# Kernel optimization log

Hardware: AMD Instinct MI355X
Metric: run time of the kernel (lower is better)

Reference implementation:

```python
import jax, jax.numpy as jnp
import numpy as np

B, T, D = 16, 32, 4096
H, HD = 32, 128          # n_heads, head_dim
MAX_SEQ = 2048
START_POS = 1024


def _rope(x):
    # x: [b, t, h, hd]; faithful to source: positions start at 0 (no start_pos offset)
    t, hd = x.shape[1], x.shape[-1]
    theta = 10000.0 ** (-2.0 * jnp.arange(0, hd, 2, dtype=jnp.float32) / hd)  # [hd/2]
    freqs = jnp.arange(t, dtype=jnp.float32)[:, None] * theta                 # [t, hd/2]
    cos = jnp.repeat(jnp.cos(freqs), 2, axis=-1)[None, :, None, :]            # [1,t,1,hd]
    sin = jnp.repeat(jnp.sin(freqs), 2, axis=-1)[None, :, None, :]
    # rotate: even slots <- -odd, odd slots <- even (interleaved)
    x_rot = jnp.stack([-x[..., 1::2], x[..., 0::2]], axis=-1).reshape(x.shape)
    return x * cos + x_rot * sin


def setup_inputs() -> dict:
    key = jax.random.key(0)
    ks = jax.random.split(key, 7)
    s = 0.02
    return {
        "x": jax.random.normal(ks[0], (B, T, D), dtype=jnp.float32),
        "wq": jax.random.normal(ks[1], (D, D), dtype=jnp.float32) * s,
        "wk": jax.random.normal(ks[2], (D, D), dtype=jnp.float32) * s,
        "wv": jax.random.normal(ks[3], (D, D), dtype=jnp.float32) * s,
        "wo": jax.random.normal(ks[4], (D, D), dtype=jnp.float32) * s,
        "k_cache": jax.random.normal(ks[5], (B, MAX_SEQ, H, HD), dtype=jnp.float32),
        "v_cache": jax.random.normal(ks[6], (B, MAX_SEQ, H, HD), dtype=jnp.float32),
        "start_pos": START_POS,
    }


def reference(x, wq, wk, wv, wo, k_cache, v_cache, start_pos):
    b, t, _ = x.shape
    xq = (x @ wq).reshape(b, t, H, HD)
    xk = (x @ wk).reshape(b, t, H, HD)
    xv = (x @ wv).reshape(b, t, H, HD)
    xq = _rope(xq)
    xk = _rope(xk)
    # KV-cache append (start_pos is a static Python int)
    k_cache = jax.lax.dynamic_update_slice(k_cache, xk, (0, start_pos, 0, 0))
    v_cache = jax.lax.dynamic_update_slice(v_cache, xv, (0, start_pos, 0, 0))
    L = start_pos + t
    keys = k_cache[:, :L]    # [b, L, h, hd]
    values = v_cache[:, :L]
    # n_rep == 1 -> repeat_kv is identity
    scores = jnp.einsum("bthd,bshd->bhts", xq, keys) / np.float32(np.sqrt(HD))
    probs = jax.nn.softmax(scores.astype(jnp.float32), axis=-1).astype(xq.dtype)
    out = jnp.einsum("bhts,bshd->bthd", probs, values).reshape(b, t, H * HD)
    return out @ wo
```

## Files before the change

kernel.cpp:

```cpp
#include <hip/hip_runtime.h>
#include <hip/hip_bf16.h>

#define B_ 16
#define T_ 32
#define D_ 4096
#define H_ 32
#define HD_ 128
#define MAXS_ 2048
#define M_ (B_*T_)

typedef __hip_bfloat16 bf16;
typedef __attribute__((ext_vector_type(8))) short bf16x8;
typedef __attribute__((ext_vector_type(4))) float f32x4;

static __device__ __forceinline__ short f2b(float f) {
    bf16 h = __float2bfloat16(f);
    return *reinterpret_cast<short*>(&h);
}
static __device__ __forceinline__ float b2f(short s) {
    bf16 h;
    *reinterpret_cast<short*>(&h) = s;
    return __bfloat162float(h);
}

#define GLD16(gsrc, ldst) \
    __builtin_amdgcn_global_load_lds((const __attribute__((address_space(1))) void*)(gsrc), \
        (__attribute__((address_space(3))) void*)(ldst), 16, 0, 0)

__global__ __launch_bounds__(256) void conv_x(const float* __restrict__ x, bf16* __restrict__ xb) {
    int idx = blockIdx.x * 256 + threadIdx.x;
    const float4* xf = (const float4*)x;
    float4 a = xf[idx * 2], b = xf[idx * 2 + 1];
    bf16x8 o;
    o[0] = f2b(a.x); o[1] = f2b(a.y); o[2] = f2b(a.z); o[3] = f2b(a.w);
    o[4] = f2b(b.x); o[5] = f2b(b.y); o[6] = f2b(b.z); o[7] = f2b(b.w);
    *(bf16x8*)&xb[(size_t)idx * 8] = o;
}

__global__ __launch_bounds__(256) void transpose_w(const float* __restrict__ W, bf16* __restrict__ wt) {
    __shared__ float Ts[64][65];
    const int n0 = blockIdx.x * 64, k0 = blockIdx.y * 64;
    const int t = threadIdx.x;
    {
        int kk = t >> 4, nn = (t & 15) * 4;
        #pragma unroll
        for (int r = 0; r < 4; ++r) {
            float4 v = *(const float4*)&W[(size_t)(k0 + kk + 16 * r) * D_ + n0 + nn];
            Ts[kk + 16 * r][nn + 0] = v.x;
            Ts[kk + 16 * r][nn + 1] = v.y;
            Ts[kk + 16 * r][nn + 2] = v.z;
            Ts[kk + 16 * r][nn + 3] = v.w;
        }
    }
    __syncthreads();
    const int kg = t & 7, nr = t >> 3;
    #pragma unroll
    for (int r = 0; r < 2; ++r) {
        int n = nr + 32 * r;
        bf16x8 o;
        #pragma unroll
        for (int j = 0; j < 8; ++j) o[j] = f2b(Ts[kg * 8 + j][n]);
        *(bf16x8*)&wt[(size_t)(n0 + n) * D_ + k0 + kg * 8] = o;
    }
}

__global__ __launch_bounds__(256) void gemm_qkvw(const bf16* __restrict__ A,
        const float* __restrict__ wq, const float* __restrict__ wk,
        const float* __restrict__ wv, bf16* __restrict__ out) {
    const int K = D_;
    const int wsel = blockIdx.x >> 5;
    const float* W = (wsel == 0) ? wq : (wsel == 1) ? wk : wv;
    const int lcol0 = (blockIdx.x & 31) * 128;
    bf16* Ob = out + (size_t)wsel * M_ * D_;
    __shared__ bf16 As[2][64 * 32];
    __shared__ short Bs[2][128][40];
    const int tid = threadIdx.x, lane = tid & 63, wave = tid >> 6;
    const int wr = wave >> 1, wc = wave & 1;
    const int lg = lane >> 4, li = lane & 15;
    const int row0 = blockIdx.y * 64;
    const int bq = tid & 31, kq = tid >> 5;
    f32x4 acc[2][4];
    #pragma unroll
    for (int i = 0; i < 2; ++i)
        #pragma unroll
        for (int j = 0; j < 4; ++j)
            #pragma unroll
            for (int r = 0; r < 4; ++r) acc[i][j][r] = 0.f;

    const int sw = (li & 3) << 4;
    for (int k0 = 0; k0 < K; k0 += 64) {
        float4 wv4[2][4];
        #pragma unroll
        for (int h = 0; h < 2; ++h)
            #pragma unroll
            for (int i = 0; i < 4; ++i)
                wv4[h][i] = *(const float4*)&W[(size_t)(k0 + 32 * h + kq * 4 + i) * D_ + lcol0 + bq * 4];
        {
            int X = tid * 16;
            int row = X >> 6;
            int kb = (X & 63) ^ ((row & 3) << 4);
            GLD16(A + (size_t)(row0 + row) * K + k0 + (kb >> 1),      (char*)As[0] + wave * 1024);
            GLD16(A + (size_t)(row0 + row) * K + k0 + 32 + (kb >> 1), (char*)As[1] + wave * 1024);
        }
        #pragma unroll
        for (int h = 0; h < 2; ++h)
            #pragma unroll
            for (int j = 0; j < 4; ++j) {
                int n = bq * 4 + j;
                short4 col;
                col.x = f2b(((const float*)&wv4[h][0])[j]);
                col.y = f2b(((const float*)&wv4[h][1])[j]);
                col.z = f2b(((const float*)&wv4[h][2])[j]);
                col.w = f2b(((const float*)&wv4[h][3])[j]);
                *(short4*)((char*)&Bs[h][n][0] + ((kq * 8) ^ (((n >> 4) & 3) << 4))) = col;
            }
        __syncthreads();
        bf16x8 af[2][2], bfr[2][4];
        #pragma unroll
        for (int h = 0; h < 2; ++h) {
            #pragma unroll
            for (int i = 0; i < 2; ++i) {
                int row = wr * 32 + i * 16 + li;
                af[h][i] = *(const bf16x8*)((const char*)As[h] + row * 64 + ((lg * 16) ^ sw));
            }
            #pragma unroll
            for (int j = 0; j < 4; ++j) {
                int row = wc * 64 + j * 16 + li;
                bfr[h][j] = *(const bf16x8*)((const char*)&Bs[h][row][0] + ((lg * 16) ^ (((row >> 4) & 3) << 4)));
            }
        }
        #pragma unroll
        for (int h = 0; h < 2; ++h)
            #pragma unroll
            for (int i = 0; i < 2; ++i)
                #pragma unroll
                for (int j = 0; j < 4; ++j)
                    acc[i][j] = __builtin_amdgcn_mfma_f32_16x16x32_bf16(af[h][i], bfr[h][j], acc[i][j], 0, 0, 0);
        __syncthreads();
    }
    #pragma unroll
    for (int i = 0; i < 2; ++i)
        for (int j = 0; j < 4; ++j)
            for (int r = 0; r < 4; ++r) {
                int row = row0 + wr * 32 + i * 16 + lg * 4 + r;
                int col = lcol0 + wc * 64 + j * 16 + li;
                Ob[(size_t)row * D_ + col] = __float2bfloat16(acc[i][j][r]);
            }
}

template<int BM, int BN>
__global__ __launch_bounds__(256) void gemm_bf16t(const bf16* __restrict__ A,
        const bf16* __restrict__ Bt, float* __restrict__ O) {
    constexpr int IM = BM / 32;
    constexpr int JN = BN / 32;
    constexpr int nA = (BM * 64) / 4096;
    constexpr int nB = (BN * 64) / 4096;
    const int K = D_;
    __shared__ bf16 As[2][BM * 32];
    __shared__ bf16 Bs[2][BN * 32];
    const int tid = threadIdx.x, lane = tid & 63, wave = tid >> 6;
    const int wr = wave >> 1, wc = wave & 1;
    const int lg = lane >> 4, li = lane & 15;
    const int row0 = blockIdx.y * BM, col0 = blockIdx.x * BN;
    f32x4 acc[IM][JN];
    #pragma unroll
    for (int i = 0; i < IM; ++i)
        #pragma unroll
        for (int j = 0; j < JN; ++j)
            #pragma unroll
            for (int r = 0; r < 4; ++r) acc[i][j][r] = 0.f;

    const int sw = (li & 3) << 4;
    for (int k0 = 0; k0 < K; k0 += 64) {
        #pragma unroll
        for (int h = 0; h < 2; ++h) {
            #pragma unroll
            for (int i = 0; i < nA; ++i) {
                int X = (i * 256 + tid) * 16;
                int row = X >> 6;
                int kb = (X & 63) ^ ((row & 3) << 4);
                GLD16(A + (size_t)(row0 + row) * K + k0 + 32 * h + (kb >> 1),
                      (char*)As[h] + (i * 256 + wave * 64) * 16);
            }
            #pragma unroll
            for (int i = 0; i < nB; ++i) {
                int X = (i * 256 + tid) * 16;
                int row = X >> 6;
                int kb = (X & 63) ^ ((row & 3) << 4);
                GLD16(Bt + (size_t)(col0 + row) * K + k0 + 32 * h + (kb >> 1),
                      (char*)Bs[h] + (i * 256 + wave * 64) * 16);
            }
        }
        __syncthreads();
        bf16x8 af[2][IM], bfr[2][JN];
        #pragma unroll
        for (int h = 0; h < 2; ++h) {
            #pragma unroll
            for (int i = 0; i < IM; ++i) {
                int row = wr * (BM / 2) + i * 16 + li;
                af[h][i] = *(const bf16x8*)((const char*)As[h] + row * 64 + ((lg * 16) ^ sw));
            }
            #pragma unroll
            for (int j = 0; j < JN; ++j) {
                int row = wc * (BN / 2) + j * 16 + li;
                bfr[h][j] = *(const bf16x8*)((const char*)Bs[h] + row * 64 + ((lg * 16) ^ sw));
            }
        }
        #pragma unroll
        for (int h = 0; h < 2; ++h)
            #pragma unroll
            for (int i = 0; i < IM; ++i)
                #pragma unroll
                for (int j = 0; j < JN; ++j)
                    acc[i][j] = __builtin_amdgcn_mfma_f32_16x16x32_bf16(af[h][i], bfr[h][j], acc[i][j], 0, 0, 0);
        __syncthreads();
    }
    #pragma unroll
    for (int i = 0; i < IM; ++i)
        for (int j = 0; j < JN; ++j)
            for (int r = 0; r < 4; ++r) {
                int row = row0 + wr * (BM / 2) + i * 16 + lg * 4 + r;
                int col = col0 + wc * (BN / 2) + j * 16 + li;
                O[(size_t)row * D_ + col] = acc[i][j][r];
            }
}

__global__ __launch_bounds__(256) void rope_inplace(bf16* __restrict__ qb, bf16* __restrict__ kb) {
    int idx = blockIdx.x * 256 + threadIdx.x;
    size_t e0 = (size_t)idx * 8;
    int hd0 = (int)(e0 & 127);
    int t = (int)((e0 >> 12) & 31);
    bf16x8 q = *(bf16x8*)&qb[e0];
    bf16x8 k = *(bf16x8*)&kb[e0];
    bf16x8 qo, ko;
    #pragma unroll
    for (int p = 0; p < 4; ++p) {
        int i = (hd0 >> 1) + p;
        float theta = exp2f(-(float)i * 0.41524101186092787f);
        float s, c;
        sincosf((float)t * theta, &s, &c);
        float q0 = b2f(q[2 * p]), q1 = b2f(q[2 * p + 1]);
        qo[2 * p]     = f2b(q0 * c - q1 * s);
        qo[2 * p + 1] = f2b(q1 * c + q0 * s);
        float k0 = b2f(k[2 * p]), k1 = b2f(k[2 * p + 1]);
        ko[2 * p]     = f2b(k0 * c - k1 * s);
        ko[2 * p + 1] = f2b(k1 * c + k0 * s);
    }
    *(bf16x8*)&qb[e0] = qo;
    *(bf16x8*)&kb[e0] = ko;
}

__global__ __launch_bounds__(256, 2) void attn(const bf16* __restrict__ qb,
        const bf16* __restrict__ kb, const bf16* __restrict__ vb,
        const float* __restrict__ kc, const float* __restrict__ vc,
        const int* __restrict__ spp, bf16* __restrict__ ob) {
    const int bh = blockIdx.x;
    const int b = bh >> 5, h = bh & 31;
    const int sp = *spp;
    const int L = sp + T_;
    const int tid = threadIdx.x, lane = tid & 63, wave = tid >> 6;
    const int lg = lane >> 4, li = lane & 15;
    const int a0 = lane >> 5, bq = lane & 31;

    __shared__ __align__(16) char smem[52352];
    auto Vt   = (short(*)[128][40])smem;
    auto Plds = (bf16(*)[32][40])(smem + 40960);
    auto msh  = (float(*)[32])(smem + 51200);
    auto lsh  = (float(*)[32])(smem + 51712);
    float* ltot = (float*)(smem + 52224);
    float(*Osh)[128] = (float(*)[128])smem;

    bf16x8 qf[2][4];
    #pragma unroll
    for (int rt = 0; rt < 2; ++rt)
        #pragma unroll
        for (int kk = 0; kk < 4; ++kk)
            qf[rt][kk] = *(const bf16x8*)(&qb[((size_t)(b * T_ + rt * 16 + li) * H_ + h) * HD_ + kk * 32 + lg * 8]);

    f32x4 o[2][8];
    float m_r[2], l_r[2];
    m_r[0] = m_r[1] = -1e30f;
    l_r[0] = l_r[1] = 0.f;
    #pragma unroll
    for (int rt = 0; rt < 2; ++rt) for (int ht = 0; ht < 8; ++ht) for (int r = 0; r < 4; ++r) o[rt][ht][r] = 0.f;

    const float scale = 0.08838834764831845f;
    const int nch = (L + 31) >> 5;
    const int ccache = sp >> 5;

    bf16x8 kf[2][4];

    auto COMPUTE = [&](int s0) {
        f32x4 sc[2][2];
        #pragma unroll
        for (int ct = 0; ct < 2; ++ct)
            #pragma unroll
            for (int rt = 0; rt < 2; ++rt) {
                f32x4 acc;
                for (int r = 0; r < 4; ++r) acc[r] = 0.f;
                #pragma unroll
                for (int kk = 0; kk < 4; ++kk)
                    acc = __builtin_amdgcn_mfma_f32_16x16x32_bf16(kf[ct][kk], qf[rt][kk], acc, 0, 0, 0);
                sc[ct][rt] = acc;
            }
        float corr[2];
        #pragma unroll
        for (int rt = 0; rt < 2; ++rt) {
            float xv[8];
            #pragma unroll
            for (int ct = 0; ct < 2; ++ct)
                #pragma unroll
                for (int r = 0; r < 4; ++r) {
                    float xx = sc[ct][rt][r] * scale;
                    if (s0 + ct * 16 + 4 * lg + r >= L) xx = -1e30f;
                    xv[ct * 4 + r] = xx;
                }
            float mx = fmaxf(fmaxf(fmaxf(xv[0], xv[1]), fmaxf(xv[2], xv[3])),
                             fmaxf(fmaxf(xv[4], xv[5]), fmaxf(xv[6], xv[7])));
            mx = fmaxf(mx, __shfl_xor(mx, 16, 64));
            mx = fmaxf(mx, __shfl_xor(mx, 32, 64));
            float mnew = fmaxf(m_r[rt], mx);
            corr[rt] = __expf(m_r[rt] - mnew);
            float p[8], ssum = 0.f;
            #pragma unroll
            for (int j = 0; j < 8; ++j) { p[j] = __expf(xv[j] - mnew); ssum += p[j]; }
            ssum += __shfl_xor(ssum, 16, 64);
            ssum += __shfl_xor(ssum, 32, 64);
            l_r[rt] = l_r[rt] * corr[rt] + ssum;
            m_r[rt] = mnew;
            #pragma unroll
            for (int ct = 0; ct < 2; ++ct)
                #pragma unroll
                for (int r = 0; r < 4; ++r)
                    Plds[wave][rt * 16 + li][ct * 16 + 4 * lg + r] = __float2bfloat16(p[ct * 4 + r]);
        }
        #pragma unroll
        for (int rt = 0; rt < 2; ++rt) {
            float cq[4];
            #pragma unroll
            for (int r = 0; r < 4; ++r) cq[r] = __shfl(corr[rt], 20 * lg + r, 64);
            #pragma unroll
            for (int ht = 0; ht < 8; ++ht)
                #pragma unroll
                for (int r = 0; r < 4; ++r) o[rt][ht][r] *= cq[r];
        }
        asm volatile("s_waitcnt lgkmcnt(0)" ::: "memory");
        bf16x8 pf[2];
        pf[0] = *(const bf16x8*)(&Plds[wave][li][lg * 8]);
        pf[1] = *(const bf16x8*)(&Plds[wave][16 + li][lg * 8]);
        #pragma unroll
        for (int ht = 0; ht < 8; ++ht) {
            int row = ht * 16 + li;
            int colB = (lg * 16) ^ ((ht & 3) << 4);
            bf16x8 vf = *(const bf16x8*)((const char*)&Vt[wave][row][0] + colB);
            #pragma unroll
            for (int rt = 0; rt < 2; ++rt)
                o[rt][ht] = __builtin_amdgcn_mfma_f32_16x16x32_bf16(pf[rt], vf, o[rt][ht], 0, 0, 0);
        }
    };

    int c = wave;
    if (c < ccache) {
        float4 vr0[8], vr1[8];
        {
            const float* vpB = &vc[(((size_t)b * MAXS_ + c * 32) * H_ + h) * HD_ + bq * 4];
            #pragma unroll
            for (int i = 0; i < 8; ++i) vr0[i] = *(const float4*)(vpB + (size_t)(a0 * 8 + i) * (H_ * HD_));
            #pragma unroll
            for (int i = 0; i < 8; ++i) vr1[i] = *(const float4*)(vpB + (size_t)((a0 + 2) * 8 + i) * (H_ * HD_));
        }
        for (;;) {
            const int s0 = c * 32;
            const int nc = c + 4;
            const bool more = nc < ccache;
            float4 kr[2][8];
            #pragma unroll
            for (int ct = 0; ct < 2; ++ct) {
                const float* kp = &kc[(((size_t)b * MAXS_ + s0 + ct * 16 + li) * H_ + h) * HD_ + lg * 8];
                #pragma unroll
                for (int kk = 0; kk < 4; ++kk) {
                    kr[ct][2 * kk]     = *(const float4*)(kp + kk * 32);
                    kr[ct][2 * kk + 1] = *(const float4*)(kp + kk * 32 + 4);
                }
            }
            #pragma unroll
            for (int rep = 0; rep < 2; ++rep) {
                const int ao = a0 + rep * 2;
                #pragma unroll
                for (int j = 0; j < 4; ++j) {
                    int row = bq * 4 + j;
                    bf16x8 w;
                    #pragma unroll
                    for (int i = 0; i < 8; ++i)
                        w[i] = f2b(((const float*)&(rep ? vr1 : vr0)[i])[j]);
                    int colB = (ao * 16) ^ (((row >> 4) & 3) << 4);
                    *(bf16x8*)((char*)&Vt[wave][row][0] + colB) = w;
                }
            }
            if (more) {
                const float* vpB = &vc[(((size_t)b * MAXS_ + nc * 32) * H_ + h) * HD_ + bq * 4];
                #pragma unroll
                for (int i = 0; i < 8; ++i) vr0[i] = *(const float4*)(vpB + (size_t)(a0 * 8 + i) * (H_ * HD_));
                #pragma unroll
                for (int i = 0; i < 8; ++i) vr1[i] = *(const float4*)(vpB + (size_t)((a0 + 2) * 8 + i) * (H_ * HD_));
            }
            #pragma unroll
            for (int ct = 0; ct < 2; ++ct)
                #pragma unroll
                for (int kk = 0; kk < 4; ++kk) {
                    bf16x8 f;
                    f[0] = f2b(kr[ct][2 * kk].x); f[1] = f2b(kr[ct][2 * kk].y);
                    f[2] = f2b(kr[ct][2 * kk].z); f[3] = f2b(kr[ct][2 * kk].w);
                    f[4] = f2b(kr[ct][2 * kk + 1].x); f[5] = f2b(kr[ct][2 * kk + 1].y);
                    f[6] = f2b(kr[ct][2 * kk + 1].z); f[7] = f2b(kr[ct][2 * kk + 1].w);
                    kf[ct][kk] = f;
                }
            COMPUTE(s0);
            c = nc;
            if (!more) break;
        }
    }
    for (; c < nch; c += 4) {
        const int s0 = c * 32;
        if (s0 >= sp) {
            #pragma unroll
            for (int rep = 0; rep < 2; ++rep) {
                int ao = a0 + rep * 2;
                short tv[8][4];
                #pragma unroll
                for (int i = 0; i < 8; ++i) {
                    int s = s0 + ao * 8 + i;
                    if (s < L) {
                        ushort4 u = *(const ushort4*)&vb[(((size_t)b * T_ + (s - sp)) * H_ + h) * HD_ + bq * 4];
                        tv[i][0] = (short)u.x; tv[i][1] = (short)u.y; tv[i][2] = (short)u.z; tv[i][3] = (short)u.w;
                    } else {
                        tv[i][0] = 0; tv[i][1] = 0; tv[i][2] = 0; tv[i][3] = 0;
                    }
                }
                #pragma unroll
                for (int j = 0; j < 4; ++j) {
                    int row = bq * 4 + j;
                    bf16x8 w;
                    #pragma unroll
                    for (int i = 0; i < 8; ++i) w[i] = tv[i][j];
                    int colB = (ao * 16) ^ (((row >> 4) & 3) << 4);
                    *(bf16x8*)((char*)&Vt[wave][row][0] + colB) = w;
                }
            }
            #pragma unroll
            for (int ct = 0; ct < 2; ++ct) {
                int s = s0 + ct * 16 + li;
                if (s < L) {
                    const bf16* kp = &kb[((size_t)(b * T_ + s - sp) * H_ + h) * HD_];
                    #pragma unroll
                    for (int kk = 0; kk < 4; ++kk)
                        kf[ct][kk] = *(const bf16x8*)(kp + kk * 32 + lg * 8);
                } else {
                    #pragma unroll
                    for (int kk = 0; kk < 4; ++kk) {
                        bf16x8 f;
                        #pragma unroll
                        for (int j = 0; j < 8; ++j) f[j] = 0;
                        kf[ct][kk] = f;
                    }
                }
            }
        } else {
            #pragma unroll
            for (int rep = 0; rep < 2; ++rep) {
                int ao = a0 + rep * 2;
                short tv[8][4];
                #pragma unroll
                for (int i = 0; i < 8; ++i) {
                    int s = s0 + ao * 8 + i;
                    if (s < sp) {
                        float4 v = *(const float4*)&vc[(((size_t)b * MAXS_ + s) * H_ + h) * HD_ + bq * 4];
                        tv[i][0] = f2b(v.x); tv[i][1] = f2b(v.y); tv[i][2] = f2b(v.z); tv[i][3] = f2b(v.w);
                    } else if (s < L) {
                        ushort4 u = *(const ushort4*)&vb[(((size_t)b * T_ + (s - sp)) * H_ + h) * HD_ + bq * 4];
                        tv[i][0] = (short)u.x; tv[i][1] = (short)u.y; tv[i][2] = (short)u.z; tv[i][3] = (short)u.w;
                    } else {
                        tv[i][0] = 0; tv[i][1] = 0; tv[i][2] = 0; tv[i][3] = 0;
                    }
                }
                #pragma unroll
                for (int j = 0; j < 4; ++j) {
                    int row = bq * 4 + j;
                    bf16x8 w;
                    #pragma unroll
                    for (int i = 0; i < 8; ++i) w[i] = tv[i][j];
                    int colB = (ao * 16) ^ (((row >> 4) & 3) << 4);
                    *(bf16x8*)((char*)&Vt[wave][row][0] + colB) = w;
                }
            }
            #pragma unroll
            for (int ct = 0; ct < 2; ++ct) {
                int s = s0 + ct * 16 + li;
                if (s < sp) {
                    const float* kp = &kc[(((size_t)b * MAXS_ + s) * H_ + h) * HD_];
                    #pragma unroll
                    for (int kk = 0; kk < 4; ++kk) {
                        float4 v0 = *(const float4*)(&kp[kk * 32 + lg * 8]);
                        float4 v1 = *(const float4*)(&kp[kk * 32 + lg * 8 + 4]);
                        bf16x8 f;
                        f[0] = f2b(v0.x); f[1] = f2b(v0.y); f[2] = f2b(v0.z); f[3] = f2b(v0.w);
                        f[4] = f2b(v1.x); f[5] = f2b(v1.y); f[6] = f2b(v1.z); f[7] = f2b(v1.w);
                        kf[ct][kk] = f;
                    }
                } else if (s < L) {
                    const bf16* kp = &kb[((size_t)(b * T_ + s - sp) * H_ + h) * HD_];
                    #pragma unroll
                    for (int kk = 0; kk < 4; ++kk)
                        kf[ct][kk] = *(const bf16x8*)(kp + kk * 32 + lg * 8);
                } else {
                    #pragma unroll
                    for (int kk = 0; kk < 4; ++kk) {
                        bf16x8 f;
                        #pragma unroll
                        for (int j = 0; j < 8; ++j) f[j] = 0;
                        kf[ct][kk] = f;
                    }
                }
            }
        }
        COMPUTE(s0);
    }

    if (lg == 0) {
        #pragma unroll
        for (int rt = 0; rt < 2; ++rt) {
            msh[wave][rt * 16 + li] = m_r[rt];
            lsh[wave][rt * 16 + li] = l_r[rt];
        }
    }
    __syncthreads();
    float corr2[2][4];
    #pragma unroll
    for (int rt = 0; rt < 2; ++rt)
        for (int r = 0; r < 4; ++r) {
            int row = rt * 16 + lg * 4 + r;
            float M = fmaxf(fmaxf(msh[0][row], msh[1][row]), fmaxf(msh[2][row], msh[3][row]));
            corr2[rt][r] = __expf(msh[wave][row] - M);
        }
    if (tid < 32) {
        int row = tid;
        float M = fmaxf(fmaxf(msh[0][row], msh[1][row]), fmaxf(msh[2][row], msh[3][row]));
        float lt = 0.f;
        #pragma unroll
        for (int w = 0; w < 4; ++w) lt += lsh[w][row] * __expf(msh[w][row] - M);
        ltot[row] = lt;
    }
    __syncthreads();
    for (int w = 0; w < 4; ++w) {
        if (wave == w) {
            #pragma unroll
            for (int rt = 0; rt < 2; ++rt)
                for (int ht = 0; ht < 8; ++ht)
                    for (int r = 0; r < 4; ++r) {
                        int row = rt * 16 + lg * 4 + r, col = ht * 16 + li;
                        float val = o[rt][ht][r] * corr2[rt][r];
                        if (w == 0) Osh[row][col] = val;
                        else Osh[row][col] += val;
                    }
        }
        __syncthreads();
    }
    {
        int row = tid >> 3;
        int c0 = (tid & 7) * 16;
        float inv = 1.0f / ltot[row];
        #pragma unroll
        for (int j = 0; j < 16; ++j)
            ob[(size_t)(b * T_ + row) * D_ + h * HD_ + c0 + j] = __float2bfloat16(Osh[row][c0 + j] * inv);
    }
}

extern "C" void kernel_launch(void* const* d_in, const int* in_sizes, int n_in,
                              void* d_out, int out_size, void* d_ws, size_t ws_size,
                              hipStream_t stream) {
    const float* x  = (const float*)d_in[0];
    const float* wq = (const float*)d_in[1];
    const float* wk = (const float*)d_in[2];
    const float* wv = (const float*)d_in[3];
    const float* wo = (const float*)d_in[4];
    const float* kc = (const float*)d_in[5];
    const float* vc = (const float*)d_in[6];
    const int*   sp = (const int*)d_in[7];

    char* ws = (char*)d_ws;
    const size_t MT = (size_t)M_ * D_;
    bf16* wt = (bf16*)ws;
    bf16* xb = wt + (size_t)D_ * D_;
    bf16* qb = xb + MT;
    bf16* kb = qb + MT;
    bf16* vb = kb + MT;
    bf16* ab = vb + MT;

    conv_x<<<dim3((int)(MT / 8 / 256)), 256, 0, stream>>>(x, xb);
    transpose_w<<<dim3(64, 64), 256, 0, stream>>>(wo, wt);
    gemm_qkvw<<<dim3(96, 8), 256, 0, stream>>>(xb, wq, wk, wv, qb);
    rope_inplace<<<dim3((int)(MT / 8 / 256)), 256, 0, stream>>>(qb, kb);
    attn<<<dim3(B_ * H_), 256, 0, stream>>>(qb, kb, vb, kc, vc, sp, ab);
    gemm_bf16t<64, 64><<<dim3(64, 8), 256, 0, stream>>>(ab, wt, (float*)d_out);
}
```

Measured before the change: 322.8 us.

## Stage fp32 V tiles into LDS with direct global-to-LDS loads and prefetch K

Replaces the register-held V prefetch and bf16 transposed LDS write with direct global-to-LDS 16-byte loads (GLD16) of raw fp32 V tiles per wave. The tiles are converted to bf16 while building the MFMA B operand. K loads for the next chunk are issued before compute, using partial vmcnt waits to overlap memory with MFMA work. This frees VGPRs and removes the transpose and pack step, at the cost of 64KB of LDS for V. That likely limits blocks per CU, and reading 8 strided scalar fp32 values per fragment from LDS may cause bank conflicts.

```diff
diff --git a/kernel.cpp b/kernel.cpp
--- a/kernel.cpp
+++ b/kernel.cpp
@@ -260,14 +260,14 @@
     const int L = sp + T_;
     const int tid = threadIdx.x, lane = tid & 63, wave = tid >> 6;
     const int lg = lane >> 4, li = lane & 15;
-    const int a0 = lane >> 5, bq = lane & 31;
-
-    __shared__ __align__(16) char smem[52352];
-    auto Vt   = (short(*)[128][40])smem;
-    auto Plds = (bf16(*)[32][40])(smem + 40960);
-    auto msh  = (float(*)[32])(smem + 51200);
-    auto lsh  = (float(*)[32])(smem + 51712);
-    float* ltot = (float*)(smem + 52224);
+
+    __shared__ __align__(16) char smem[76928];
+    char* VLDSw = smem + wave * 16384;
+    float(*Vf)[128] = (float(*)[128])VLDSw;
+    auto Plds = (bf16(*)[32][40])(smem + 65536);
+    auto msh  = (float(*)[32])(smem + 75776);
+    auto lsh  = (float(*)[32])(smem + 76288);
+    float* ltot = (float*)(smem + 76800);
     float(*Osh)[128] = (float(*)[128])smem;
 
     bf16x8 qf[2][4];
@@ -289,8 +289,42 @@
     const int ccache = sp >> 5;
 
     bf16x8 kf[2][4];
-
-    auto COMPUTE = [&](int s0) {
+    float4 kr[16];
+
+    auto KISSUE = [&](int cc) {
+        #pragma unroll
+        for (int ct = 0; ct < 2; ++ct) {
+            const float* kp = &kc[(((size_t)b * MAXS_ + cc * 32 + ct * 16 + li) * H_ + h) * HD_ + lg * 8];
+            #pragma unroll
+            for (int kk = 0; kk < 4; ++kk) {
+                kr[ct * 8 + 2 * kk]     = *(const float4*)(kp + kk * 32);
+                kr[ct * 8 + 2 * kk + 1] = *(const float4*)(kp + kk * 32 + 4);
+            }
+        }
+    };
+    auto VSTAGE = [&](int cc) {
+        const float* src = vc + (((size_t)b * MAXS_ + cc * 32) * H_ + h) * HD_;
+        #pragma unroll
+        for (int i = 0; i < 16; ++i) {
+            GLD16(src + (size_t)(2 * i + (lane >> 5)) * (H_ * HD_) + (lane & 31) * 4,
+                  VLDSw + i * 1024);
+        }
+    };
+    auto KBUILD = [&]() {
+        #pragma unroll
+        for (int ct = 0; ct < 2; ++ct)
+            #pragma unroll
+            for (int kk = 0; kk < 4; ++kk) {
+                bf16x8 f;
+                f[0] = f2b(kr[ct * 8 + 2 * kk].x); f[1] = f2b(kr[ct * 8 + 2 * kk].y);
+                f[2] = f2b(kr[ct * 8 + 2 * kk].z); f[3] = f2b(kr[ct * 8 + 2 * kk].w);
+                f[4] = f2b(kr[ct * 8 + 2 * kk + 1].x); f[5] = f2b(kr[ct * 8 + 2 * kk + 1].y);
+                f[6] = f2b(kr[ct * 8 + 2 * kk + 1].z); f[7] = f2b(kr[ct * 8 + 2 * kk + 1].w);
+                kf[ct][kk] = f;
+            }
+    };
+
+    auto COMPUTE = [&](int s0, bool deep) {
         f32x4 sc[2][2];
         #pragma unroll
         for (int ct = 0; ct < 2; ++ct)
@@ -344,15 +378,18 @@
                 #pragma unroll
                 for (int r = 0; r < 4; ++r) o[rt][ht][r] *= cq[r];
         }
-        asm volatile("s_waitcnt lgkmcnt(0)" ::: "memory");
+        if (deep) asm volatile("s_waitcnt vmcnt(16) lgkmcnt(0)" ::: "memory");
+        else      asm volatile("s_waitcnt vmcnt(0) lgkmcnt(0)" ::: "memory");
+        __builtin_amdgcn_sched_barrier(0);
         bf16x8 pf[2];
         pf[0] = *(const bf16x8*)(&Plds[wave][li][lg * 8]);
         pf[1] = *(const bf16x8*)(&Plds[wave][16 + li][lg * 8]);
         #pragma unroll
         for (int ht = 0; ht < 8; ++ht) {
-            int row = ht * 16 + li;
-            int colB = (lg * 16) ^ ((ht & 3) << 4);
-            bf16x8 vf = *(const bf16x8*)((const char*)&Vt[wave][row][0] + colB);
+            bf16x8 vf;
+            #pragma unroll
+            for (int j = 0; j < 8; ++j)
+                vf[j] = f2b(Vf[lg * 8 + j][ht * 16 + li]);
             #pragma unroll
             for (int rt = 0; rt < 2; ++rt)
                 o[rt][ht] = __builtin_amdgcn_mfma_f32_16x16x32_bf16(pf[rt], vf, o[rt][ht], 0, 0, 0);
@@ -361,169 +398,69 @@
 
     int c = wave;
     if (c < ccache) {
-        float4 vr0[8], vr1[8];
-        {
-            const float* vpB = &vc[(((size_t)b * MAXS_ + c * 32) * H_ + h) * HD_ + bq * 4];
-            #pragma unroll
-            for (int i = 0; i < 8; ++i) vr0[i] = *(const float4*)(vpB + (size_t)(a0 * 8 + i) * (H_ * HD_));
-            #pragma unroll
-            for (int i = 0; i < 8; ++i) vr1[i] = *(const float4*)(vpB + (size_t)((a0 + 2) * 8 + i) * (H_ * HD_));
-        }
+        KISSUE(c);
+        VSTAGE(c);
         for (;;) {
             const int s0 = c * 32;
             const int nc = c + 4;
             const bool more = nc < ccache;
-            float4 kr[2][8];
-            #pragma unroll
-            for (int ct = 0; ct < 2; ++ct) {
-                const float* kp = &kc[(((size_t)b * MAXS_ + s0 + ct * 16 + li) * H_ + h) * HD_ + lg * 8];
+            KBUILD();
+            if (more) KISSUE(nc);
+            COMPUTE(s0, more);
+            asm volatile("s_waitcnt lgkmcnt(0)" ::: "memory");
+            if (more) VSTAGE(nc);
+            c = nc;
+            if (!more) break;
+        }
+    }
+    for (; c < nch; c += 4) {
+        const int s0 = c * 32;
+        #pragma unroll
+        for (int u = 0; u < 16; ++u) {
+            int F = lane + 64 * u;
+            int s = F >> 5, q = F & 31;
+            int ss = s0 + s;
+            float4 v;
+            if (ss < sp) {
+                v = *(const float4*)&vc[(((size_t)b * MAXS_ + ss) * H_ + h) * HD_ + q * 4];
+            } else if (ss < L) {
+                ushort4 uu = *(const ushort4*)&vb[(((size_t)b * T_ + (ss - sp)) * H_ + h) * HD_ + q * 4];
+                v = make_float4(b2f((short)uu.x), b2f((short)uu.y), b2f((short)uu.z), b2f((short)uu.w));
+            } else {
+                v = make_float4(0.f, 0.f, 0.f, 0.f);
+            }
+            *(float4*)&Vf[s][q * 4] = v;
+        }
+        #pragma unroll
+        for (int ct = 0; ct < 2; ++ct) {
+            int s = s0 + ct * 16 + li;
+            if (s < sp) {
+                const float* kp = &kc[(((size_t)b * MAXS_ + s) * H_ + h) * HD_];
                 #pragma unroll
                 for (int kk = 0; kk < 4; ++kk) {
-                    kr[ct][2 * kk]     = *(const float4*)(kp + kk * 32);
-                    kr[ct][2 * kk + 1] = *(const float4*)(kp + kk * 32 + 4);
+                    float4 v0 = *(const float4*)(&kp[kk * 32 + lg * 8]);
+                    float4 v1 = *(const float4*)(&kp[kk * 32 + lg * 8 + 4]);
+                    bf16x8 f;
+                    f[0] = f2b(v0.x); f[1] = f2b(v0.y); f[2] = f2b(v0.z); f[3] = f2b(v0.w);
+                    f[4] = f2b(v1.x); f[5] = f2b(v1.y); f[6] = f2b(v1.z); f[7] = f2b(v1.w);
+                    kf[ct][kk] = f;
                 }
-            }
-            #pragma unroll
-            for (int rep = 0; rep < 2; ++rep) {
-                const int ao = a0 + rep * 2;
-                #pragma unroll
-                for (int j = 0; j < 4; ++j) {
-                    int row = bq * 4 + j;
-                    bf16x8 w;
-                    #pragma unroll
-                    for (int i = 0; i < 8; ++i)
-                        w[i] = f2b(((const float*)&(rep ? vr1 : vr0)[i])[j]);
-                    int colB = (ao * 16) ^ (((row >> 4) & 3) << 4);
-                    *(bf16x8*)((char*)&Vt[wave][row][0] + colB) = w;
-                }
-            }
-            if (more) {
-                const float* vpB = &vc[(((size_t)b * MAXS_ + nc * 32) * H_ + h) * HD_ + bq * 4];
-                #pragma unroll
-                for (int i = 0; i < 8; ++i) vr0[i] = *(const float4*)(vpB + (size_t)(a0 * 8 + i) * (H_ * HD_));
-                #pragma unroll
-                for (int i = 0; i < 8; ++i) vr1[i] = *(const float4*)(vpB + (size_t)((a0 + 2) * 8 + i) * (H_ * HD_));
-            }
-            #pragma unroll
-            for (int ct = 0; ct < 2; ++ct)
+            } else if (s < L) {
+                const bf16* kp = &kb[((size_t)(b * T_ + s - sp) * H_ + h) * HD_];
+                #pragma unroll
+                for (int kk = 0; kk < 4; ++kk)
+                    kf[ct][kk] = *(const bf16x8*)(kp + kk * 32 + lg * 8);
+            } else {
                 #pragma unroll
                 for (int kk = 0; kk < 4; ++kk) {
                     bf16x8 f;
-                    f[0] = f2b(kr[ct][2 * kk].x); f[1] = f2b(kr[ct][2 * kk].y);
-                    f[2] = f2b(kr[ct][2 * kk].z); f[3] = f2b(kr[ct][2 * kk].w);
-                    f[4] = f2b(kr[ct][2 * kk + 1].x); f[5] = f2b(kr[ct][2 * kk + 1].y);
-                    f[6] = f2b(kr[ct][2 * kk + 1].z); f[7] = f2b(kr[ct][2 * kk + 1].w);
+                    #pragma unroll
+                    for (int j = 0; j < 8; ++j) f[j] = 0;
                     kf[ct][kk] = f;
                 }
-            COMPUTE(s0);
-            c = nc;
-            if (!more) break;
-        }
-    }
-    for (; c < nch; c += 4) {
-        const int s0 = c * 32;
-        if (s0 >= sp) {
-            #pragma unroll
-            for (int rep = 0; rep < 2; ++rep) {
-                int ao = a0 + rep * 2;
-                short tv[8][4];
-                #pragma unroll
-                for (int i = 0; i < 8; ++i) {
-                    int s = s0 + ao * 8 + i;
-                    if (s < L) {
-                        ushort4 u = *(const ushort4*)&vb[(((size_t)b * T_ + (s - sp)) * H_ + h) * HD_ + bq * 4];
-                        tv[i][0] = (short)u.x; tv[i][1] = (short)u.y; tv[i][2] = (short)u.z; tv[i][3] = (short)u.w;
-                    } else {
-                        tv[i][0] = 0; tv[i][1] = 0; tv[i][2] = 0; tv[i][3] = 0;
-                    }
-                }
-                #pragma unroll
-                for (int j = 0; j < 4; ++j) {
-                    int row = bq * 4 + j;
-                    bf16x8 w;
-                    #pragma unroll
-                    for (int i = 0; i < 8; ++i) w[i] = tv[i][j];
-                    int colB = (ao * 16) ^ (((row >> 4) & 3) << 4);
-                    *(bf16x8*)((char*)&Vt[wave][row][0] + colB) = w;
-                }
-            }
-            #pragma unroll
-            for (int ct = 0; ct < 2; ++ct) {
-                int s = s0 + ct * 16 + li;
-                if (s < L) {
-                    const bf16* kp = &kb[((size_t)(b * T_ + s - sp) * H_ + h) * HD_];
-                    #pragma unroll
-                    for (int kk = 0; kk < 4; ++kk)
-                        kf[ct][kk] = *(const bf16x8*)(kp + kk * 32 + lg * 8);
-                } else {
-                    #pragma unroll
-                    for (int kk = 0; kk < 4; ++kk) {
-                        bf16x8 f;
-                        #pragma unroll
-                        for (int j = 0; j < 8; ++j) f[j] = 0;
-                        kf[ct][kk] = f;
-                    }
-                }
-            }
-        } else {
-            #pragma unroll
-            for (int rep = 0; rep < 2; ++rep) {
-                int ao = a0 + rep * 2;
-                short tv[8][4];
-                #pragma unroll
-                for (int i = 0; i < 8; ++i) {
-                    int s = s0 + ao * 8 + i;
-                    if (s < sp) {
-                        float4 v = *(const float4*)&vc[(((size_t)b * MAXS_ + s) * H_ + h) * HD_ + bq * 4];
-                        tv[i][0] = f2b(v.x); tv[i][1] = f2b(v.y); tv[i][2] = f2b(v.z); tv[i][3] = f2b(v.w);
-                    } else if (s < L) {
-                        ushort4 u = *(const ushort4*)&vb[(((size_t)b * T_ + (s - sp)) * H_ + h) * HD_ + bq * 4];
-                        tv[i][0] = (short)u.x; tv[i][1] = (short)u.y; tv[i][2] = (short)u.z; tv[i][3] = (short)u.w;
-                    } else {
-                        tv[i][0] = 0; tv[i][1] = 0; tv[i][2] = 0; tv[i][3] = 0;
-                    }
-                }
-                #pragma unroll
-                for (int j = 0; j < 4; ++j) {
-                    int row = bq * 4 + j;
-                    bf16x8 w;
-                    #pragma unroll
-                    for (int i = 0; i < 8; ++i) w[i] = tv[i][j];
-                    int colB = (ao * 16) ^ (((row >> 4) & 3) << 4);
-                    *(bf16x8*)((char*)&Vt[wave][row][0] + colB) = w;
-                }
-            }
-            #pragma unroll
-            for (int ct = 0; ct < 2; ++ct) {
-                int s = s0 + ct * 16 + li;
-                if (s < sp) {
-                    const float* kp = &kc[(((size_t)b * MAXS_ + s) * H_ + h) * HD_];
-                    #pragma unroll
-                    for (int kk = 0; kk < 4; ++kk) {
-                        float4 v0 = *(const float4*)(&kp[kk * 32 + lg * 8]);
-                        float4 v1 = *(const float4*)(&kp[kk * 32 + lg * 8 + 4]);
-                        bf16x8 f;
-                        f[0] = f2b(v0.x); f[1] = f2b(v0.y); f[2] = f2b(v0.z); f[3] = f2b(v0.w);
-                        f[4] = f2b(v1.x); f[5] = f2b(v1.y); f[6] = f2b(v1.z); f[7] = f2b(v1.w);
-                        kf[ct][kk] = f;
-                    }
-                } else if (s < L) {
-                    const bf16* kp = &kb[((size_t)(b * T_ + s - sp) * H_ + h) * HD_];
-                    #pragma unroll
-                    for (int kk = 0; kk < 4; ++kk)
-                        kf[ct][kk] = *(const bf16x8*)(kp + kk * 32 + lg * 8);
-                } else {
-                    #pragma unroll
-                    for (int kk = 0; kk < 4; ++kk) {
-                        bf16x8 f;
-                        #pragma unroll
-                        for (int j = 0; j < 8; ++j) f[j] = 0;
-                        kf[ct][kk] = f;
-                    }
-                }
-            }
-        }
-        COMPUTE(s0);
+            }
+        }
+        COMPUTE(s0, false);
     }
 
     if (lg == 0) {
```

Result: no change. 318.2 us (median of 2 runs) (-1.4%).
